# Performance work log

Measured on AMD Instinct MI355X. Metric: run time of the kernel, lower is better.

## Reference

```python
import jax, jax.numpy as jnp
import numpy as np

EPS = 1e-08


def setup_inputs() -> dict:
    key = jax.random.key(0)
    k1, k2 = jax.random.split(key)
    z = jax.random.normal(k1, (32, 768, 32, 32), dtype=jnp.float32)
    memory = jax.random.normal(k2, (512, 768), dtype=jnp.float32)
    return {"z": z, "memory": memory}


def _l2_normalize(x, axis=-1, eps=1e-12):
    # Matches torch F.normalize(dim=-1): x / max(||x||, eps)
    n = jnp.sqrt(jnp.sum(x * x, axis=axis, keepdims=True))
    return x / jnp.maximum(n, eps)


def reference(z, memory):
    B, C, H, W = z.shape
    M = memory.shape[0]
    # (B, C, H, W) -> (B, H*W, C)
    z_flat = jnp.transpose(z, (0, 2, 3, 1)).reshape(B, H * W, C)
    z_norm = _l2_normalize(z_flat)
    mem_norm = _l2_normalize(memory)
    # cosine-similarity scores: (B, N, M)
    scores = jnp.einsum('bnc,mc->bnm', z_norm, mem_norm)
    w = jax.nn.softmax(scores, axis=-1)
    lam = 1.0 / M
    # hard-shrink sparsification: relu(w - lam) * w / (|w - lam| + eps)
    d = w - lam
    attn_w = jax.nn.relu(d) * w / (jnp.abs(d) + EPS)
    attn_w = attn_w / (jnp.sum(attn_w, axis=-1, keepdims=True) + EPS)
    # weighted readout against the RAW (un-normalized) memory
    z_hat_flat = jnp.einsum('bnm,mc->bnc', attn_w, memory)
    z_hat = jnp.transpose(z_hat_flat.reshape(B, H, W, C), (0, 3, 1, 2))
    return (z_hat, attn_w)
```

## Files before the change

kernel.cpp:

```cpp
#include <hip/hip_runtime.h>
#include <hip/hip_bf16.h>
#include <math.h>

typedef short short8 __attribute__((ext_vector_type(8)));
typedef float f32x4 __attribute__((ext_vector_type(4)));
typedef _Float16 f16x8 __attribute__((ext_vector_type(8)));

#define CC 768
#define NN 1024
#define RR 32768
#define MM 512
#define ZSTRIDE 786432
#define OUT_ATTN_OFF 25165824
#define SPLIT_SC 2048.0f
#define INV_SC   (1.0f / 2048.0f)

static __device__ __forceinline__ short f2bf(float f) {
    __hip_bfloat16 h = __float2bfloat16(f);
    return *reinterpret_cast<short*>(&h);
}

static __device__ __forceinline__ double fast_exp_neg(double x) {
    const double LOG2E = 1.4426950408889634074;
    const double LN2   = 0.6931471805599453094;
    const double MAGIC = 6755399441055744.0;
    double t = x * LOG2E;
    double c = t + MAGIC;
    double n = c - MAGIC;
    int ni = (int)__double2loint(c);
    double g = (t - n) * LN2;
    double r = 2.505210838544172e-08;
    r = fma(r, g, 2.755731922398589e-07);
    r = fma(r, g, 2.7557319223985893e-06);
    r = fma(r, g, 2.48015873015873e-05);
    r = fma(r, g, 1.984126984126984e-04);
    r = fma(r, g, 1.388888888888889e-03);
    r = fma(r, g, 8.333333333333333e-03);
    r = fma(r, g, 4.1666666666666664e-02);
    r = fma(r, g, 1.6666666666666666e-01);
    r = fma(r, g, 0.5);
    r = fma(r, g, 1.0);
    r = fma(r, g, 1.0);
    double sc = __hiloint2double((1023 + ni) << 20, 0);
    return r * sc;
}

static __device__ __forceinline__ double fast_rcp(double x) {
    double r = (double)(1.0f / (float)x);
    r = r * (2.0 - x * r);
    r = r * (2.0 - x * r);
    return r;
}

__global__ __launch_bounds__(256) void prep_mem_kernel(const float* __restrict__ memory,
                                                       _Float16* __restrict__ mem_h,
                                                       _Float16* __restrict__ mem_L,
                                                       short* __restrict__ memT_bf) {
    int m = blockIdx.x;
    int t = threadIdx.x;
    double ss = 0.0;
    for (int c = t; c < CC; c += 256) {
        float v = memory[m * CC + c];
        ss += (double)v * (double)v;
    }
    #pragma unroll
    for (int off = 32; off > 0; off >>= 1) ss += __shfl_xor(ss, off);
    __shared__ double red[4];
    __shared__ double invs;
    if ((t & 63) == 0) red[t >> 6] = ss;
    __syncthreads();
    if (t == 0) {
        double tot = red[0] + red[1] + red[2] + red[3];
        invs = 1.0 / fmax(sqrt(tot), 1e-12);
    }
    __syncthreads();
    float inv = (float)invs;
    for (int c = t; c < CC; c += 256) {
        float v  = memory[m * CC + c];
        float nv = v * inv;
        _Float16 h = (_Float16)nv;
        float r1 = nv - (float)h;
        mem_h[m * CC + c] = h;
        mem_L[m * CC + c] = (_Float16)(r1 * SPLIT_SC);
        memT_bf[c * MM + m] = f2bf(v);
    }
}

#define SWZ(row_, k_) ((((row_) << 5) + (k_)) ^ (((row_) & 7) << 3))
__global__ __launch_bounds__(512, 4) void scores_gemm_kernel(const float* __restrict__ z,
                                                             const _Float16* __restrict__ mem_h,
                                                             const _Float16* __restrict__ mem_L,
                                                             float* __restrict__ out_scores,
                                                             double* __restrict__ zinv_ws) {
    __shared__ _Float16 AT[2][2][4096];
    __shared__ _Float16 BT[2][2][4096];
    __shared__ double ssred[512];

    const int t    = threadIdx.x;
    const int lane = t & 63;
    const int wv   = t >> 6;
    const int lrow = lane & 15;
    const int gk   = lane >> 4;
    const int wr   = wv >> 1, wc = wv & 1;
    const int d = blockIdx.x;
    const int colblk = (d >> 3) & 3;
    const int rowblk = (d & 7) | ((d >> 5) << 3);
    const int row0 = rowblk * 128;
    const int b    = row0 >> 10;
    const int n0   = row0 & 1023;
    const int cB0  = colblk * 128;

    const int an  = t & 127;
    const int ak8 = (t >> 7) * 8;
    const float* zA = z + (size_t)b * ZSTRIDE + n0 + an;

    const int br0 = ((t >> 2) ^ (t >> 4)) & 1;
    const int br  = ((t >> 3) << 1) | br0;
    const int bk8 = (((t & 3) ^ ((((t >> 3) & 1) << 1) | br0)) << 3);
    const _Float16* srcBh = mem_h + (size_t)(cB0 + br) * CC + bk8;
    const _Float16* srcBL = mem_L + (size_t)(cB0 + br) * CC + bk8;

    double ss = 0.0;
    f32x4 am[2][4], ax[2][4];
    #pragma unroll
    for (int fc = 0; fc < 2; ++fc)
        #pragma unroll
        for (int fn = 0; fn < 4; ++fn) {
            am[fc][fn] = (f32x4){0.f, 0.f, 0.f, 0.f};
            ax[fc][fn] = (f32x4){0.f, 0.f, 0.f, 0.f};
        }

    float avX[8], avY[8];

    #define DMA_B(bb_, kt_)                                                    \
        do {                                                                   \
            __builtin_amdgcn_global_load_lds(                                  \
                (const __attribute__((address_space(1))) void*)(srcBh + (kt_) * 32), \
                (__attribute__((address_space(3))) void*)(&BT[bb_][0][wv * 512]),    \
                16, 0, 0);                                                     \
            __builtin_amdgcn_global_load_lds(                                  \
                (const __attribute__((address_space(1))) void*)(srcBL + (kt_) * 32), \
                (__attribute__((address_space(3))) void*)(&BT[bb_][1][wv * 512]),    \
                16, 0, 0);                                                     \
        } while (0)

    #define LOAD_A(kt_, av_)                                                   \
        do {                                                                   \
            _Pragma("unroll")                                                  \
            for (int j = 0; j < 8; ++j)                                        \
                av_[j] = zA[(size_t)((kt_) * 32 + ak8 + j) * NN];              \
        } while (0)

    #define WRITE_A(bb_, av_)                                                  \
        do {                                                                   \
            f16x8 h8, l8;                                                      \
            _Pragma("unroll")                                                  \
            for (int j = 0; j < 8; ++j) {                                      \
                float v = av_[j];                                              \
                ss = fma((double)v, (double)v, ss);                            \
                _Float16 h = (_Float16)v;                                      \
                h8[j] = h;                                                     \
                l8[j] = (_Float16)((v - (float)h) * SPLIT_SC);                 \
            }                                                                  \
            *reinterpret_cast<f16x8*>(&AT[bb_][0][SWZ(an, ak8)]) = h8;         \
            *reinterpret_cast<f16x8*>(&AT[bb_][1][SWZ(an, ak8)]) = l8;         \
        } while (0)

    #define MFMA_BLOCK(cur_)                                                       \
        do {                                                                       \
            f16x8 ah0 = *reinterpret_cast<const f16x8*>(                           \
                &AT[cur_][0][SWZ(wr * 32 + lrow, gk * 8)]);                        \
            f16x8 ah1 = *reinterpret_cast<const f16x8*>(                           \
                &AT[cur_][0][SWZ(wr * 32 + 16 + lrow, gk * 8)]);                   \
            f16x8 aL0 = *reinterpret_cast<const f16x8*>(                           \
                &AT[cur_][1][SWZ(wr * 32 + lrow, gk * 8)]);                        \
            f16x8 aL1 = *reinterpret_cast<const f16x8*>(                           \
                &AT[cur_][1][SWZ(wr * 32 + 16 + lrow, gk * 8)]);                   \
            _Pragma("unroll")                                                      \
            for (int fn = 0; fn < 4; ++fn) {                                       \
                f16x8 bhf = *reinterpret_cast<const f16x8*>(                       \
                    &BT[cur_][0][SWZ(wc * 64 + fn * 16 + lrow, gk * 8)]);          \
                f16x8 bLf = *reinterpret_cast<const f16x8*>(                       \
                    &BT[cur_][1][SWZ(wc * 64 + fn * 16 + lrow, gk * 8)]);          \
                am[0][fn] = __builtin_amdgcn_mfma_f32_16x16x32_f16(ah0, bhf, am[0][fn], 0, 0, 0); \
                ax[0][fn] = __builtin_amdgcn_mfma_f32_16x16x32_f16(aL0, bhf, ax[0][fn], 0, 0, 0); \
                ax[0][fn] = __builtin_amdgcn_mfma_f32_16x16x32_f16(ah0, bLf, ax[0][fn], 0, 0, 0); \
                am[1][fn] = __builtin_amdgcn_mfma_f32_16x16x32_f16(ah1, bhf, am[1][fn], 0, 0, 0); \
                ax[1][fn] = __builtin_amdgcn_mfma_f32_16x16x32_f16(aL1, bhf, ax[1][fn], 0, 0, 0); \
                ax[1][fn] = __builtin_amdgcn_mfma_f32_16x16x32_f16(ah1, bLf, ax[1][fn], 0, 0, 0); \
            }                                                                      \
        } while (0)

    DMA_B(0, 0);
    LOAD_A(0, avX);
    WRITE_A(0, avX);
    LOAD_A(1, avY);
    __syncthreads();

    #pragma unroll 1
    for (int kt = 0; kt < 24; kt += 2) {
        if (kt + 1 < 24) DMA_B(1, kt + 1);
        if (kt + 2 < 24) LOAD_A(kt + 2, avX);
        MFMA_BLOCK(0);
        if (kt + 1 < 24) WRITE_A(1, avY);
        __syncthreads();
        if (kt + 2 < 24) DMA_B(0, kt + 2);
        if (kt + 3 < 24) LOAD_A(kt + 3, avY);
        MFMA_BLOCK(1);
        if (kt + 2 < 24) WRITE_A(0, avX);
        __syncthreads();
    }
    #undef DMA_B
    #undef LOAD_A
    #undef WRITE_A
    #undef MFMA_BLOCK

    #pragma unroll
    for (int fc = 0; fc < 2; ++fc)
        #pragma unroll
        for (int fn = 0; fn < 4; ++fn)
            #pragma unroll
            for (int rg = 0; rg < 4; ++rg) {
                int row = row0 + wr * 32 + fc * 16 + gk * 4 + rg;
                int col = cB0 + wc * 64 + fn * 16 + lrow;
                out_scores[(size_t)row * MM + col] = am[fc][fn][rg] + ax[fc][fn][rg] * INV_SC;
            }

    ssred[t] = ss;
    __syncthreads();
    if (colblk == 0 && t < 128) {
        double tot = ssred[t] + ssred[t + 128] + ssred[t + 256] + ssred[t + 384];
        zinv_ws[row0 + t] = 1.0 / fmax(sqrt(tot), 1e-12);
    }
}

__global__ __launch_bounds__(256) void epilogue_kernel(float* __restrict__ attn,
                                                       const double* __restrict__ zinv_ws) {
    const int t    = threadIdx.x;
    const int lane = t & 63;
    const int wv   = t >> 6;
    const int row0 = blockIdx.x * 64;

    #pragma unroll 1
    for (int i = 0; i < 16; ++i) {
        int row = row0 + wv * 16 + i;
        double zi = zinv_ws[row];
        float* rp = attn + (size_t)row * MM;
        f32x4 x0 = *reinterpret_cast<const f32x4*>(&rp[lane * 4]);
        f32x4 x1 = *reinterpret_cast<const f32x4*>(&rp[256 + lane * 4]);
        double s0 = (double)x0[0] * zi, s1 = (double)x0[1] * zi;
        double s2 = (double)x0[2] * zi, s3 = (double)x0[3] * zi;
        double s4 = (double)x1[0] * zi, s5 = (double)x1[1] * zi;
        double s6 = (double)x1[2] * zi, s7 = (double)x1[3] * zi;
        double mx = fmax(fmax(fmax(s0, s1), fmax(s2, s3)),
                         fmax(fmax(s4, s5), fmax(s6, s7)));
        #pragma unroll
        for (int off = 32; off > 0; off >>= 1) mx = fmax(mx, __shfl_xor(mx, off));
        double p0 = fast_exp_neg(s0 - mx), p1 = fast_exp_neg(s1 - mx);
        double p2 = fast_exp_neg(s2 - mx), p3 = fast_exp_neg(s3 - mx);
        double p4 = fast_exp_neg(s4 - mx), p5 = fast_exp_neg(s5 - mx);
        double p6 = fast_exp_neg(s6 - mx), p7 = fast_exp_neg(s7 - mx);
        double Z = ((p0 + p1) + (p2 + p3)) + ((p4 + p5) + (p6 + p7));
        #pragma unroll
        for (int off = 32; off > 0; off >>= 1) Z += __shfl_xor(Z, off);
        double iZ = fast_rcp(Z);
        const double LAM = 1.0 / 512.0;
        double w0 = p0 * iZ, w1 = p1 * iZ, w2 = p2 * iZ, w3 = p3 * iZ;
        double w4 = p4 * iZ, w5 = p5 * iZ, w6 = p6 * iZ, w7 = p7 * iZ;
        double d0 = w0 - LAM, d1 = w1 - LAM, d2 = w2 - LAM, d3 = w3 - LAM;
        double d4 = w4 - LAM, d5 = w5 - LAM, d6 = w6 - LAM, d7 = w7 - LAM;
        double e0 = (d0 > 0.0 ? d0 : 0.0) * w0 * fast_rcp(fabs(d0) + 1e-8);
        double e1 = (d1 > 0.0 ? d1 : 0.0) * w1 * fast_rcp(fabs(d1) + 1e-8);
        double e2 = (d2 > 0.0 ? d2 : 0.0) * w2 * fast_rcp(fabs(d2) + 1e-8);
        double e3 = (d3 > 0.0 ? d3 : 0.0) * w3 * fast_rcp(fabs(d3) + 1e-8);
        double e4 = (d4 > 0.0 ? d4 : 0.0) * w4 * fast_rcp(fabs(d4) + 1e-8);
        double e5 = (d5 > 0.0 ? d5 : 0.0) * w5 * fast_rcp(fabs(d5) + 1e-8);
        double e6 = (d6 > 0.0 ? d6 : 0.0) * w6 * fast_rcp(fabs(d6) + 1e-8);
        double e7 = (d7 > 0.0 ? d7 : 0.0) * w7 * fast_rcp(fabs(d7) + 1e-8);
        double S = ((e0 + e1) + (e2 + e3)) + ((e4 + e5) + (e6 + e7));
        #pragma unroll
        for (int off = 32; off > 0; off >>= 1) S += __shfl_xor(S, off);
        double rinv = fast_rcp(S + 1e-8);
        f32x4 o0 = { (float)(e0 * rinv), (float)(e1 * rinv),
                     (float)(e2 * rinv), (float)(e3 * rinv) };
        f32x4 o1 = { (float)(e4 * rinv), (float)(e5 * rinv),
                     (float)(e6 * rinv), (float)(e7 * rinv) };
        *reinterpret_cast<f32x4*>(&rp[lane * 4])       = o0;
        *reinterpret_cast<f32x4*>(&rp[256 + lane * 4]) = o1;
    }
}

__global__ __launch_bounds__(256, 3) void readout_kernel(const short* __restrict__ memT_bf,
                                                         const float* __restrict__ attn,
                                                         float* __restrict__ out) {
    __shared__ short At[2][4096];
    __shared__ short Bt[2][4096];
    const int t = threadIdx.x;
    const int d  = blockIdx.x;
    const int xs = d & 7;
    const int hi = d >> 3;
    const int c0idx  = hi % 6;
    const int rowmid = hi / 6;
    const int rb     = xs | (rowmid << 3);
    const int c0     = c0idx * 128;
    const int rowblk = rb * 128;
    const int b  = rowblk >> 10;
    const int nb = rowblk & 1023;
    const int lane = t & 63, wv = t >> 6;
    const int wcr = wv >> 1, wcc = wv & 1;
    const int lrow = lane & 15, gk = lane >> 4;

    f32x4 acc[4][4];
    #pragma unroll
    for (int fc = 0; fc < 4; ++fc)
        #pragma unroll
        for (int fn = 0; fn < 4; ++fn) acc[fc][fn] = (f32x4){0.f, 0.f, 0.f, 0.f};

    int ar[2], ak[2];
    #pragma unroll
    for (int i = 0; i < 2; ++i) {
        int u = i * 256 + t;
        int r0 = ((u >> 2) ^ (u >> 4)) & 1;
        ar[i] = ((u >> 3) << 1) | r0;
        ak[i] = ((u & 3) ^ ((((u >> 3) & 1) << 1) | r0)) << 3;
    }
    const int sr = t >> 1;
    const int ko = (t & 1) * 16;
    const float* attnB = attn + (size_t)(rowblk + sr) * MM + ko;

    #define RSWZ(row_, k_) ((((row_) << 5) + (k_)) ^ (((row_) & 7) << 3))

    #define DMA_A(bb_, m0_)                                                    \
        do {                                                                   \
            __builtin_amdgcn_global_load_lds(                                  \
                (const __attribute__((address_space(1))) void*)                \
                    (memT_bf + (size_t)(c0 + ar[0]) * MM + (m0_) + ak[0]),     \
                (__attribute__((address_space(3))) void*)(&At[bb_][wv * 512]), \
                16, 0, 0);                                                     \
            __builtin_amdgcn_global_load_lds(                                  \
                (const __attribute__((address_space(1))) void*)                \
                    (memT_bf + (size_t)(c0 + ar[1]) * MM + (m0_) + ak[1]),     \
                (__attribute__((address_space(3))) void*)(&At[bb_][2048 + wv * 512]), \
                16, 0, 0);                                                     \
        } while (0)

    #define LOAD_B(m0_, v_)                                                    \
        do {                                                                   \
            const f32x4* src = reinterpret_cast<const f32x4*>(attnB + (m0_));  \
            v_[0] = src[0]; v_[1] = src[1]; v_[2] = src[2]; v_[3] = src[3];    \
        } while (0)

    #define WRITE_B(bb_, v_)                                                   \
        do {                                                                   \
            short8 s0 = { f2bf(v_[0][0]), f2bf(v_[0][1]), f2bf(v_[0][2]), f2bf(v_[0][3]), \
                          f2bf(v_[1][0]), f2bf(v_[1][1]), f2bf(v_[1][2]), f2bf(v_[1][3]) }; \
            short8 s1 = { f2bf(v_[2][0]), f2bf(v_[2][1]), f2bf(v_[2][2]), f2bf(v_[2][3]), \
                          f2bf(v_[3][0]), f2bf(v_[3][1]), f2bf(v_[3][2]), f2bf(v_[3][3]) }; \
            *reinterpret_cast<short8*>(&Bt[bb_][RSWZ(sr, ko)])     = s0;       \
            *reinterpret_cast<short8*>(&Bt[bb_][RSWZ(sr, ko + 8)]) = s1;       \
        } while (0)

    #define MFMA_STEP(bb_)                                                     \
        do {                                                                   \
            short8 af[4], bf[4];                                               \
            _Pragma("unroll")                                                  \
            for (int fc = 0; fc < 4; ++fc)                                     \
                af[fc] = *reinterpret_cast<const short8*>(                     \
                    &At[bb_][RSWZ(wcr * 64 + fc * 16 + lrow, gk * 8)]);        \
            _Pragma("unroll")                                                  \
            for (int fn = 0; fn < 4; ++fn)                                     \
                bf[fn] = *reinterpret_cast<const short8*>(                     \
                    &Bt[bb_][RSWZ(wcc * 64 + fn * 16 + lrow, gk * 8)]);        \
            _Pragma("unroll")                                                  \
            for (int fc = 0; fc < 4; ++fc)                                     \
                _Pragma("unroll")                                              \
                for (int fn = 0; fn < 4; ++fn)                                 \
                    acc[fc][fn] = __builtin_amdgcn_mfma_f32_16x16x32_bf16(     \
                        af[fc], bf[fn], acc[fc][fn], 0, 0, 0);                 \
        } while (0)

    {
        f32x4 v[4];
        DMA_A(0, 0);
        LOAD_B(0, v);
        WRITE_B(0, v);
    }
    __syncthreads();

    #pragma unroll 1
    for (int step = 0; step < 16; ++step) {
        const int cur = step & 1;
        f32x4 v[4];
        if (step < 15) {
            DMA_A(cur ^ 1, (step + 1) * 32);
            LOAD_B((step + 1) * 32, v);
        }
        MFMA_STEP(cur);
        if (step < 15) WRITE_B(cur ^ 1, v);
        __syncthreads();
    }
    #undef DMA_A
    #undef LOAD_B
    #undef WRITE_B
    #undef MFMA_STEP
    #undef RSWZ

    #pragma unroll
    for (int fc = 0; fc < 4; ++fc)
        #pragma unroll
        for (int fn = 0; fn < 4; ++fn)
            #pragma unroll
            for (int reg = 0; reg < 4; ++reg) {
                int c = c0 + wcr * 64 + fc * 16 + gk * 4 + reg;
                int n = nb + wcc * 64 + fn * 16 + lrow;
                out[(size_t)b * ZSTRIDE + (size_t)c * NN + n] = acc[fc][fn][reg];
            }
}
#undef SWZ

extern "C" void kernel_launch(void* const* d_in, const int* in_sizes, int n_in,
                              void* d_out, int out_size, void* d_ws, size_t ws_size,
                              hipStream_t stream) {
    const float* z      = (const float*)d_in[0];
    const float* memory = (const float*)d_in[1];
    float* out      = (float*)d_out;
    float* out_attn = out + OUT_ATTN_OFF;

    char* wsb = (char*)d_ws;
    _Float16* mem_h   = (_Float16*)wsb;
    _Float16* mem_L   = (_Float16*)(wsb + 786432);
    short*    memT_bf = (short*)(wsb + 1572864);
    double*   zinv_ws = (double*)(wsb + 2359296);

    prep_mem_kernel<<<512, 256, 0, stream>>>(memory, mem_h, mem_L, memT_bf);
    scores_gemm_kernel<<<1024, 512, 0, stream>>>(z, mem_h, mem_L, out_attn, zinv_ws);
    epilogue_kernel<<<RR / 64, 256, 0, stream>>>(out_attn, zinv_ws);
    readout_kernel<<<1536, 256, 0, stream>>>(memT_bf, out_attn, out);
}
```

Measured before the change: 190.6 us.

## Emit bf16 attention copy in epilogue and DMA both readout operands to LDS

The epilogue now also writes a bf16 copy of the normalized attention weights into workspace. A new readout kernel loads both the memory and attention tiles straight into LDS with global_load_lds, which removes the fp32 register loads, conversion and LDS writes from the readout loop and allows 4 blocks per CU. In exchange the epilogue writes an extra 32 MB, and the new path is used only when the workspace is large enough, otherwise the old kernel runs.

```diff
diff --git a/kernel.cpp b/kernel.cpp
--- a/kernel.cpp
+++ b/kernel.cpp
@@ -2,6 +2,7 @@
 #include <hip/hip_bf16.h>
 #include <math.h>
 
+typedef short s16x4 __attribute__((ext_vector_type(4)));
 typedef short short8 __attribute__((ext_vector_type(8)));
 typedef float f32x4 __attribute__((ext_vector_type(4)));
 typedef _Float16 f16x8 __attribute__((ext_vector_type(8)));
@@ -235,7 +236,8 @@
 }
 
 __global__ __launch_bounds__(256) void epilogue_kernel(float* __restrict__ attn,
-                                                       const double* __restrict__ zinv_ws) {
+                                                       const double* __restrict__ zinv_ws,
+                                                       short* __restrict__ attn_bf) {
     const int t    = threadIdx.x;
     const int lane = t & 63;
     const int wv   = t >> 6;
@@ -287,7 +289,118 @@
                      (float)(e6 * rinv), (float)(e7 * rinv) };
         *reinterpret_cast<f32x4*>(&rp[lane * 4])       = o0;
         *reinterpret_cast<f32x4*>(&rp[256 + lane * 4]) = o1;
-    }
+        if (attn_bf) {
+            s16x4 b0 = { f2bf(o0[0]), f2bf(o0[1]), f2bf(o0[2]), f2bf(o0[3]) };
+            s16x4 b1 = { f2bf(o1[0]), f2bf(o1[1]), f2bf(o1[2]), f2bf(o1[3]) };
+            *reinterpret_cast<s16x4*>(&attn_bf[(size_t)row * MM + lane * 4])       = b0;
+            *reinterpret_cast<s16x4*>(&attn_bf[(size_t)row * MM + 256 + lane * 4]) = b1;
+        }
+    }
+}
+
+#define RSWZ(row_, k_) ((((row_) << 5) + (k_)) ^ (((row_) & 7) << 3))
+
+__global__ __launch_bounds__(256, 4) void readout_dma_kernel(const short* __restrict__ memT_bf,
+                                                             const short* __restrict__ attn_bf,
+                                                             float* __restrict__ out) {
+    __shared__ short At[2][4096];
+    __shared__ short Bt[2][4096];
+    const int t = threadIdx.x;
+    const int d  = blockIdx.x;
+    const int xs = d & 7;
+    const int hi = d >> 3;
+    const int c0idx  = hi % 6;
+    const int rowmid = hi / 6;
+    const int rb     = xs | (rowmid << 3);
+    const int c0     = c0idx * 128;
+    const int rowblk = rb * 128;
+    const int b  = rowblk >> 10;
+    const int nb = rowblk & 1023;
+    const int lane = t & 63, wv = t >> 6;
+    const int wcr = wv >> 1, wcc = wv & 1;
+    const int lrow = lane & 15, gk = lane >> 4;
+
+    f32x4 acc[4][4];
+    #pragma unroll
+    for (int fc = 0; fc < 4; ++fc)
+        #pragma unroll
+        for (int fn = 0; fn < 4; ++fn) acc[fc][fn] = (f32x4){0.f, 0.f, 0.f, 0.f};
+
+    int ar[2], ak[2];
+    #pragma unroll
+    for (int i = 0; i < 2; ++i) {
+        int u = i * 256 + t;
+        int r0 = ((u >> 2) ^ (u >> 4)) & 1;
+        ar[i] = ((u >> 3) << 1) | r0;
+        ak[i] = ((u & 3) ^ ((((u >> 3) & 1) << 1) | r0)) << 3;
+    }
+
+    #define DMA_STEP(bb_, m0_)                                                 \
+        do {                                                                   \
+            __builtin_amdgcn_global_load_lds(                                  \
+                (const __attribute__((address_space(1))) void*)                \
+                    (memT_bf + (size_t)(c0 + ar[0]) * MM + (m0_) + ak[0]),     \
+                (__attribute__((address_space(3))) void*)(&At[bb_][wv * 512]), \
+                16, 0, 0);                                                     \
+            __builtin_amdgcn_global_load_lds(                                  \
+                (const __attribute__((address_space(1))) void*)                \
+                    (memT_bf + (size_t)(c0 + ar[1]) * MM + (m0_) + ak[1]),     \
+                (__attribute__((address_space(3))) void*)(&At[bb_][2048 + wv * 512]), \
+                16, 0, 0);                                                     \
+            __builtin_amdgcn_global_load_lds(                                  \
+                (const __attribute__((address_space(1))) void*)                \
+                    (attn_bf + (size_t)(rowblk + ar[0]) * MM + (m0_) + ak[0]), \
+                (__attribute__((address_space(3))) void*)(&Bt[bb_][wv * 512]), \
+                16, 0, 0);                                                     \
+            __builtin_amdgcn_global_load_lds(                                  \
+                (const __attribute__((address_space(1))) void*)                \
+                    (attn_bf + (size_t)(rowblk + ar[1]) * MM + (m0_) + ak[1]), \
+                (__attribute__((address_space(3))) void*)(&Bt[bb_][2048 + wv * 512]), \
+                16, 0, 0);                                                     \
+        } while (0)
+
+    #define MFMA_STEP(bb_)                                                     \
+        do {                                                                   \
+            short8 af[4], bf[4];                                               \
+            _Pragma("unroll")                                                  \
+            for (int fc = 0; fc < 4; ++fc)                                     \
+                af[fc] = *reinterpret_cast<const short8*>(                     \
+                    &At[bb_][RSWZ(wcr * 64 + fc * 16 + lrow, gk * 8)]);        \
+            _Pragma("unroll")                                                  \
+            for (int fn = 0; fn < 4; ++fn)                                     \
+                bf[fn] = *reinterpret_cast<const short8*>(                     \
+                    &Bt[bb_][RSWZ(wcc * 64 + fn * 16 + lrow, gk * 8)]);        \
+            _Pragma("unroll")                                                  \
+            for (int fc = 0; fc < 4; ++fc)                                     \
+                _Pragma("unroll")                                              \
+                for (int fn = 0; fn < 4; ++fn)                                 \
+                    acc[fc][fn] = __builtin_amdgcn_mfma_f32_16x16x32_bf16(     \
+                        af[fc], bf[fn], acc[fc][fn], 0, 0, 0);                 \
+        } while (0)
+
+    DMA_STEP(0, 0);
+    __syncthreads();
+
+    #pragma unroll 1
+    for (int step = 0; step < 16; ++step) {
+        const int cur = step & 1;
+        if (step < 15) DMA_STEP(cur ^ 1, (step + 1) * 32);
+        MFMA_STEP(cur);
+        __syncthreads();
+    }
+    #undef DMA_STEP
+    #undef MFMA_STEP
+
+    #pragma unroll
+    for (int fc = 0; fc < 4; ++fc)
+        #pragma unroll
+        for (int fn = 0; fn < 4; ++fn)
+            #pragma unroll
+            for (int reg = 0; reg < 4; ++reg) {
+                int c = c0 + wcr * 64 + fc * 16 + gk * 4 + reg;
+                int n = nb + wcc * 64 + fn * 16 + lrow;
+                out[(size_t)b * ZSTRIDE + (size_t)c * NN + n] = acc[fc][fn][reg];
+            }
 }
 
 __global__ __launch_bounds__(256, 3) void readout_kernel(const short* __restrict__ memT_bf,
@@ -328,8 +441,6 @@
     const int ko = (t & 1) * 16;
     const float* attnB = attn + (size_t)(rowblk + sr) * MM + ko;
 
-    #define RSWZ(row_, k_) ((((row_) << 5) + (k_)) ^ (((row_) & 7) << 3))
-
     #define DMA_A(bb_, m0_)                                                    \
         do {                                                                   \
             __builtin_amdgcn_global_load_lds(                                  \
@@ -403,7 +514,6 @@
     #undef LOAD_B
     #undef WRITE_B
     #undef MFMA_STEP
-    #undef RSWZ
 
     #pragma unroll
     for (int fc = 0; fc < 4; ++fc)
@@ -416,6 +526,7 @@
                 out[(size_t)b * ZSTRIDE + (size_t)c * NN + n] = acc[fc][fn][reg];
             }
 }
+#undef RSWZ
 #undef SWZ
 
 extern "C" void kernel_launch(void* const* d_in, const int* in_sizes, int n_in,
@@ -431,9 +542,16 @@
     _Float16* mem_L   = (_Float16*)(wsb + 786432);
     short*    memT_bf = (short*)(wsb + 1572864);
     double*   zinv_ws = (double*)(wsb + 2359296);
+    const size_t WS_BASE = 2621440;
+    const size_t ATTN_BF_BYTES = (size_t)RR * MM * 2;
+    short* attn_bf = (ws_size >= WS_BASE + ATTN_BF_BYTES)
+                         ? (short*)(wsb + WS_BASE) : (short*)nullptr;
 
     prep_mem_kernel<<<512, 256, 0, stream>>>(memory, mem_h, mem_L, memT_bf);
     scores_gemm_kernel<<<1024, 512, 0, stream>>>(z, mem_h, mem_L, out_attn, zinv_ws);
-    epilogue_kernel<<<RR / 64, 256, 0, stream>>>(out_attn, zinv_ws);
-    readout_kernel<<<1536, 256, 0, stream>>>(memT_bf, out_attn, out);
-}
+    epilogue_kernel<<<RR / 64, 256, 0, stream>>>(out_attn, zinv_ws, attn_bf);
+    if (attn_bf)
+        readout_dma_kernel<<<1536, 256, 0, stream>>>(memT_bf, attn_bf, out);
+    else
+        readout_kernel<<<1536, 256, 0, stream>>>(memT_bf, out_attn, out);
+}
```

After: 191.3 us. Within noise of the previous version (+0.3%).
